# Kernel optimization log

Hardware: AMD Instinct MI355X
Metric: run time of the kernel (lower is better)

Reference implementation:

```python
import jax, jax.numpy as jnp
import numpy as np

N = 100000      # nodes
E = 1000000     # edges
H_DIM = 124     # node embedding dim
CLS_DIM = 4     # node class-logit dim (H_DIM + CLS_DIM = in_features = 128)
POLAR_DIM = 2   # edge_pred_features
HIDDEN = 256
OUT = 2
LN_EPS = 1e-5


def setup_inputs() -> dict:
    key = jax.random.key(0)
    ks = jax.random.split(key, 10)
    in_dim = 2 * (H_DIM + CLS_DIM) + POLAR_DIM  # 258
    return {
        "h": jax.random.normal(ks[0], (N, H_DIM), dtype=jnp.float32),
        "cls": jax.random.normal(ks[1], (N, CLS_DIM), dtype=jnp.float32),
        "polar": jax.random.normal(ks[2], (E, POLAR_DIM), dtype=jnp.float32),
        "src": jax.random.randint(ks[3], (E,), 0, N, dtype=jnp.int64),
        "dst": jax.random.randint(ks[4], (E,), 0, N, dtype=jnp.int64),
        # parameters (PyTorch Linear default-ish init scale)
        "W1": jax.random.normal(ks[5], (in_dim, HIDDEN), dtype=jnp.float32) * (1.0 / np.sqrt(in_dim)),
        "b1": jnp.zeros((HIDDEN,), dtype=jnp.float32),
        "gamma": jnp.ones((HIDDEN,), dtype=jnp.float32),
        "beta": jnp.zeros((HIDDEN,), dtype=jnp.float32),
        "W2": jax.random.normal(ks[6], (HIDDEN, OUT), dtype=jnp.float32) * (1.0 / np.sqrt(HIDDEN)),
        "b2": jnp.zeros((OUT,), dtype=jnp.float32),
    }


def reference(h, cls, polar, src, dst, W1, b1, gamma, beta, W2, b2):
    # softmax over class logits per node (same math as softmax on gathered
    # edge copies, but computed once per node)
    cls_sm = jax.nn.softmax(cls, axis=1)                  # [N, CLS_DIM]
    # gather src/dst node features along edges
    x = jnp.concatenate(
        [h[src], cls_sm[src], polar, h[dst], cls_sm[dst]], axis=1
    )                                                     # [E, 258]
    z = x @ W1 + b1                                        # [E, HIDDEN]
    # LayerNorm
    mu = jnp.mean(z, axis=-1, keepdims=True)
    var = jnp.mean(jnp.square(z - mu), axis=-1, keepdims=True)
    z = (z - mu) * jax.lax.rsqrt(var + LN_EPS) * gamma + beta
    z = jax.nn.relu(z)
    # dropout is identity in eval mode
    score = z @ W2 + b2                                    # [E, OUT]
    return score
```

## Files before the change

### kernel.cpp

```cpp
#include <hip/hip_runtime.h>
#include <hip/hip_bf16.h>

#define NN 100000
#define EE 1000000
#define H_DIM 124
#define PCOLS 512
#define LDK 136
#define CW 132

typedef float f32x4 __attribute__((ext_vector_type(4)));
typedef unsigned int u32x4 __attribute__((ext_vector_type(4)));
typedef short bf16x8 __attribute__((ext_vector_type(8)));
typedef _Float16 h2 __attribute__((ext_vector_type(2)));

__device__ __forceinline__ unsigned short f2bf(float f) {
    unsigned int x = __float_as_uint(f);
    unsigned int r = (x + 0x7FFFu + ((x >> 16) & 1u)) >> 16;
    return (unsigned short)r;
}
__device__ __forceinline__ unsigned int pk2bf(float a, float b) {
    return (unsigned int)f2bf(a) | ((unsigned int)f2bf(b) << 16);
}
__device__ __forceinline__ unsigned int pk2h(float a, float b) {
    h2 v = (h2){(_Float16)a, (_Float16)b};
    return __builtin_bit_cast(unsigned int, v);
}

__device__ __forceinline__ float fdot2(h2 a, h2 b, float c) {
#if __has_builtin(__builtin_amdgcn_fdot2)
    return __builtin_amdgcn_fdot2(a, b, c, false);
#else
    return c + (float)a[0] * (float)b[0] + (float)a[1] * (float)b[1];
#endif
}

#if __has_builtin(__builtin_amdgcn_update_dpp)
template <int CTRL>
__device__ __forceinline__ float dpp_add(float x) {
    int xi = __builtin_bit_cast(int, x);
    int t = __builtin_amdgcn_update_dpp(xi, xi, CTRL, 0xF, 0xF, false);
    return x + __builtin_bit_cast(float, t);
}
__device__ __forceinline__ float reduce16(float x) {
    x = dpp_add<0x128>(x);
    x = dpp_add<0x124>(x);
    x = dpp_add<0x122>(x);
    x = dpp_add<0x121>(x);
    return x;
}
#else
__device__ __forceinline__ float reduce16(float x) {
    x += __shfl_xor(x, 8); x += __shfl_xor(x, 4);
    x += __shfl_xor(x, 2); x += __shfl_xor(x, 1);
    return x;
}
#endif

__global__ __launch_bounds__(256) void build_w1t_ct(const float* __restrict__ W1,
                                                    const float* __restrict__ gamma,
                                                    const float* __restrict__ beta,
                                                    const float* __restrict__ W2,
                                                    unsigned short* __restrict__ W1T,
                                                    uint4* __restrict__ CT) {
    if (blockIdx.x < 256) {
        int t2 = blockIdx.x * 256 + threadIdx.x;
        int j = t2 >> 7, k = t2 & 127;
        int row = (j < 256) ? k : (130 + k);
        int col = (j < 256) ? j : (j - 256);
        W1T[t2] = f2bf(W1[row * 256 + col]);
    } else {
        int t = threadIdx.x;
        if (t < 192) {
            int slot = t % 12, il = t / 12;
            int a = slot >> 1, k = slot & 1;
            int j0 = il * 16 + k * 8;
            float v[8];
            #pragma unroll
            for (int i = 0; i < 8; ++i) {
                int j = j0 + i;
                v[i] = (a == 0) ? W1[128 * 256 + j]
                     : (a == 1) ? W1[129 * 256 + j]
                     : (a == 2) ? gamma[j]
                     : (a == 3) ? beta[j]
                     : (a == 4) ? W2[2 * j]
                     :            W2[2 * j + 1];
            }
            CT[t] = make_uint4(pk2h(v[0], v[1]), pk2h(v[2], v[3]),
                               pk2h(v[4], v[5]), pk2h(v[6], v[7]));
        }
    }
}

__global__ __launch_bounds__(256) void p_gemm(const float* __restrict__ h,
                                              const float* __restrict__ cls,
                                              const unsigned short* __restrict__ W1T,
                                              const float* __restrict__ b1,
                                              _Float16* __restrict__ P) {
    __shared__ alignas(16) unsigned short As[64 * LDK];
    __shared__ alignas(16) unsigned short Bs[128 * LDK];
    float* Cs = (float*)&Bs[0];
    const int m0 = blockIdx.x * 64;
    const int t = threadIdx.x;

    #pragma unroll
    for (int it = 0; it < 4; ++it) {
        int chunk = t + it * 256;
        int r = chunk >> 4, c8 = chunk & 15;
        int row = m0 + r;
        unsigned int w0 = 0, w1 = 0, w2 = 0, w3 = 0;
        if (row < NN) {
            if (c8 < 15) {
                const float* hp = h + (size_t)row * H_DIM + c8 * 8;
                float4 v0 = *(const float4*)(hp);
                float4 v1 = *(const float4*)(hp + 4);
                w0 = pk2bf(v0.x, v0.y); w1 = pk2bf(v0.z, v0.w);
                w2 = pk2bf(v1.x, v1.y); w3 = pk2bf(v1.z, v1.w);
            } else {
                float4 v0 = *(const float4*)(h + (size_t)row * H_DIM + 120);
                float4 c = *(const float4*)(cls + (size_t)row * 4);
                float m = fmaxf(fmaxf(c.x, c.y), fmaxf(c.z, c.w));
                float e0 = __expf(c.x - m), e1 = __expf(c.y - m);
                float e2 = __expf(c.z - m), e3 = __expf(c.w - m);
                float inv = 1.0f / (e0 + e1 + e2 + e3);
                w0 = pk2bf(v0.x, v0.y); w1 = pk2bf(v0.z, v0.w);
                w2 = pk2bf(e0 * inv, e1 * inv); w3 = pk2bf(e2 * inv, e3 * inv);
            }
        }
        *(uint4*)(&As[r * LDK + c8 * 8]) = make_uint4(w0, w1, w2, w3);
    }
    __syncthreads();

    const int wave = t >> 6, lane = t & 63;
    const int wm = wave & 1, wn = wave >> 1;
    const int lm = lane & 15, quad = lane >> 4;

    bf16x8 afrag[4][2];
    #pragma unroll
    for (int s = 0; s < 4; ++s) {
        int k0 = s * 32 + quad * 8;
        #pragma unroll
        for (int mt = 0; mt < 2; ++mt)
            afrag[s][mt] = *(const bf16x8*)(&As[(wm * 32 + mt * 16 + lm) * LDK + k0]);
    }

    for (int cchunk = 0; cchunk < 4; ++cchunk) {
        const int n0 = cchunk * 128;
        if (cchunk) __syncthreads();
        #pragma unroll
        for (int it = 0; it < 8; ++it) {
            int chunk = t + it * 256;
            int r = chunk >> 4, c = chunk & 15;
            float4 v = *(const float4*)(W1T + (n0 + r) * 128 + c * 8);
            *(float4*)(&Bs[r * LDK + c * 8]) = v;
        }
        __syncthreads();

        f32x4 acc[2][4];
        #pragma unroll
        for (int mt = 0; mt < 2; ++mt)
            #pragma unroll
            for (int nt = 0; nt < 4; ++nt)
                acc[mt][nt] = (f32x4){0.f, 0.f, 0.f, 0.f};

        #pragma unroll
        for (int s = 0; s < 4; ++s) {
            int k0 = s * 32 + quad * 8;
            bf16x8 b[4];
            #pragma unroll
            for (int nt = 0; nt < 4; ++nt)
                b[nt] = *(const bf16x8*)(&Bs[(wn * 64 + nt * 16 + lm) * LDK + k0]);
            #pragma unroll
            for (int mt = 0; mt < 2; ++mt)
                #pragma unroll
                for (int nt = 0; nt < 4; ++nt)
                    acc[mt][nt] = __builtin_amdgcn_mfma_f32_16x16x32_bf16(afrag[s][mt], b[nt], acc[mt][nt], 0, 0, 0);
        }
        __syncthreads();

        #pragma unroll
        for (int mt = 0; mt < 2; ++mt)
            #pragma unroll
            for (int nt = 0; nt < 4; ++nt) {
                int col = wn * 64 + nt * 16 + lm;
                int rb  = wm * 32 + mt * 16 + quad * 4;
                #pragma unroll
                for (int r = 0; r < 4; ++r)
                    Cs[(rb + r) * CW + col] = acc[mt][nt][r];
            }
        __syncthreads();

        #pragma unroll
        for (int it = 0; it < 4; ++it) {
            int chunk = t + it * 256;
            int r = chunk >> 4, c8 = chunk & 15;
            float4 a = *(const float4*)(Cs + r * CW + c8 * 8);
            float4 b = *(const float4*)(Cs + r * CW + c8 * 8 + 4);
            if (n0 >= 256) {
                int cb = n0 + c8 * 8 - 256;
                float4 ba = *(const float4*)(b1 + cb);
                float4 bb = *(const float4*)(b1 + cb + 4);
                a.x += ba.x; a.y += ba.y; a.z += ba.z; a.w += ba.w;
                b.x += bb.x; b.y += bb.y; b.z += bb.z; b.w += bb.w;
            }
            uint4 o = make_uint4(pk2h(a.x, a.y), pk2h(a.z, a.w),
                                 pk2h(b.x, b.y), pk2h(b.z, b.w));
            int row = m0 + r;
            if (row < NN)
                *(uint4*)(P + (size_t)row * PCOLS + n0 + c8 * 8) = o;
        }
    }
}

#define K3_BLOCKS 4096
#define K3_STRIDE 65536
#define K3_ROUNDS 16

__device__ __forceinline__ void stage16(const void* g, void* l) {
#if __has_builtin(__builtin_amdgcn_global_load_lds)
    __builtin_amdgcn_global_load_lds((const __attribute__((address_space(1))) void*)g,
                                     (__attribute__((address_space(3))) void*)l, 16, 0, 0);
#else
    int ln = threadIdx.x & 63;
    *(uint4*)((char*)l + ln * 16) = *(const uint4*)g;
#endif
}
__device__ __forceinline__ void stage4(const void* g, void* l) {
#if __has_builtin(__builtin_amdgcn_global_load_lds)
    __builtin_amdgcn_global_load_lds((const __attribute__((address_space(1))) void*)g,
                                     (__attribute__((address_space(3))) void*)l, 4, 0, 0);
#else
    int ln = threadIdx.x & 63;
    *(unsigned*)((char*)l + ln * 4) = *(const unsigned*)g;
#endif
}

__device__ __forceinline__ h2 pick(const u32x4& x0, const u32x4& x1, int j) {
    unsigned v = (j < 4) ? x0[j] : x1[j - 4];
    return __builtin_bit_cast(h2, v);
}

__global__ __launch_bounds__(256, 4) void edge_kernel(const _Float16* __restrict__ P,
                                                      const int* __restrict__ src,
                                                      const int* __restrict__ dst,
                                                      const float* __restrict__ polar,
                                                      const uint4* __restrict__ CT,
                                                      const float* __restrict__ b2,
                                                      float* __restrict__ out) {
    __shared__ alignas(16) char SB[4 * 8192 + 4 * 768];
    const int t    = threadIdx.x;
    const int lane = t & 63;
    const int w    = t >> 6;
    const int il   = lane & 15;
    const int g    = lane >> 4;
    const int wid  = blockIdx.x * 4 + w;
    const int ebase = wid * 4;

    char* pb = SB + w * 8192;
    char* ib = SB + 4 * 8192 + w * 768;

    uint4 cq[12];
    #pragma unroll
    for (int i = 0; i < 12; ++i) cq[i] = CT[il * 12 + i];
    h2 w0c[8], w1c[8], gc[8], bc[8], w2ac[8], w2bc[8];
    {
        const h2* ch = (const h2*)cq;
        #pragma unroll
        for (int p = 0; p < 8; ++p) {
            w0c[p]  = ch[p];      w1c[p]  = ch[8 + p];
            gc[p]   = ch[16 + p]; bc[p]   = ch[24 + p];
            w2ac[p] = ch[32 + p]; w2bc[p] = ch[40 + p];
        }
    }
    const float b20 = b2[0], b21 = b2[1];
    const h2 onep  = (h2){(_Float16)1.0f, (_Float16)1.0f};
    const h2 zerop = (h2){(_Float16)0.0f, (_Float16)0.0f};

    const int sel  = (il < 4) ? 0 : (il < 8) ? 1 : 2;
    const int eoff = (il < 4) ? il : (il < 8) ? (il - 4) : ((il - 8) >> 1);
    const int comp = (sel == 2) ? (il & 1) : 0;

    #define IDX_GADDR(rr)                                                      \
        ((sel == 0) ? (const void*)(src + (((ebase + eoff + (rr) * K3_STRIDE) < EE) ? (ebase + eoff + (rr) * K3_STRIDE) : (EE - 1))) \
       : (sel == 1) ? (const void*)(dst + (((ebase + eoff + (rr) * K3_STRIDE) < EE) ? (ebase + eoff + (rr) * K3_STRIDE) : (EE - 1))) \
       :              (const void*)(polar + 2 * (size_t)(((ebase + eoff + (rr) * K3_STRIDE) < EE) ? (ebase + eoff + (rr) * K3_STRIDE) : (EE - 1)) + comp))

    stage4(IDX_GADDR(0), ib + 0);
    asm volatile("s_waitcnt vmcnt(0)" ::: "memory");
    __builtin_amdgcn_sched_barrier(0);
    {
        const unsigned* inx = (const unsigned*)(ib + 0);
        unsigned sv = inx[g], dv = inx[4 + g];
        sv = (sv < NN) ? sv : 0u; dv = (dv < NN) ? dv : 0u;
        const char* srow = (const char*)P + ((size_t)sv << 10) + il * 32;
        const char* drow = (const char*)P + ((size_t)dv << 10) + 512 + il * 32;
        stage16(srow, pb);            stage16(srow + 16, pb + 1024);
        stage16(drow, pb + 2048);     stage16(drow + 16, pb + 3072);
    }
    stage4(IDX_GADDR(1), ib + 256);

    #pragma unroll
    for (int r = 0; r < K3_ROUNDS; ++r) {
        char* pcur = pb + (r & 1) * 4096;
        const char* icur = ib + (r % 3) * 256;
        asm volatile("s_waitcnt vmcnt(0)" ::: "memory");
        __builtin_amdgcn_sched_barrier(0);

        if (r + 1 < K3_ROUNDS) {
            const unsigned* inx = (const unsigned*)(ib + ((r + 1) % 3) * 256);
            unsigned sv = inx[g], dv = inx[4 + g];
            sv = (sv < NN) ? sv : 0u; dv = (dv < NN) ? dv : 0u;
            char* pnxt = pb + ((r + 1) & 1) * 4096;
            const char* srow = (const char*)P + ((size_t)sv << 10) + il * 32;
            const char* drow = (const char*)P + ((size_t)dv << 10) + 512 + il * 32;
            stage16(srow, pnxt);          stage16(srow + 16, pnxt + 1024);
            stage16(drow, pnxt + 2048);   stage16(drow + 16, pnxt + 3072);
        }
        if (r + 2 < K3_ROUNDS)
            stage4(IDX_GADDR(r + 2), ib + ((r + 2) % 3) * 256);

        float2 qv = *(const float2*)(icur + 32 + 8 * g);
        u32x4 a0 = *(const u32x4*)(pcur + lane * 16);
        u32x4 a1 = *(const u32x4*)(pcur + 1024 + lane * 16);
        u32x4 c0 = *(const u32x4*)(pcur + 2048 + lane * 16);
        u32x4 c1 = *(const u32x4*)(pcur + 3072 + lane * 16);

        h2 p0 = (h2){(_Float16)qv.x, (_Float16)qv.x};
        h2 p1 = (h2){(_Float16)qv.y, (_Float16)qv.y};
        h2 z[8];
        float sum = 0.f, ss = 0.f;
        #pragma unroll
        for (int p = 0; p < 8; ++p) {
            h2 pv = pick(a0, a1, p) + pick(c0, c1, p);
            h2 cc = w0c[p] * p0 + w1c[p] * p1;
            z[p] = pv + cc;
            sum = fdot2(z[p], onep, sum);
            ss  = fdot2(z[p], z[p], ss);
        }
        sum = reduce16(sum); ss = reduce16(ss);
        float mu   = sum * (1.0f / 256.0f);
        float var  = ss * (1.0f / 256.0f) - mu * mu;
        float rstd = rsqrtf(var + 1e-5f);
        float nmur = -mu * rstd;
        h2 rsh = (h2){(_Float16)rstd, (_Float16)rstd};
        h2 nmh = (h2){(_Float16)nmur, (_Float16)nmur};
        float o0 = 0.f, o1 = 0.f;
        #pragma unroll
        for (int p = 0; p < 8; ++p) {
            h2 tt = z[p] * rsh + nmh;
            h2 u  = tt * gc[p] + bc[p];
            u = __builtin_elementwise_max(u, zerop);
            o0 = fdot2(u, w2ac[p], o0);
            o1 = fdot2(u, w2bc[p], o1);
        }
        o0 = reduce16(o0); o1 = reduce16(o1);
        int eg = ebase + g + r * K3_STRIDE;
        if (il == 0 && eg < EE)
            *(float2*)(out + 2 * (size_t)eg) = make_float2(o0 + b20, o1 + b21);
    }
    #undef IDX_GADDR
}

extern "C" void kernel_launch(void* const* d_in, const int* in_sizes, int n_in,
                              void* d_out, int out_size, void* d_ws, size_t ws_size,
                              hipStream_t stream) {
    const float* h     = (const float*)d_in[0];
    const float* cls   = (const float*)d_in[1];
    const float* polar = (const float*)d_in[2];
    const int*   src   = (const int*)d_in[3];
    const int*   dst   = (const int*)d_in[4];
    const float* W1    = (const float*)d_in[5];
    const float* b1    = (const float*)d_in[6];
    const float* gamma = (const float*)d_in[7];
    const float* beta  = (const float*)d_in[8];
    const float* W2    = (const float*)d_in[9];
    const float* b2    = (const float*)d_in[10];
    float* out = (float*)d_out;

    char* ws = (char*)d_ws;
    _Float16*       P   = (_Float16*)ws;
    unsigned short* W1T = (unsigned short*)(ws + 102400000);
    uint4*          CT  = (uint4*)(ws + 102531072);

    build_w1t_ct<<<257, 256, 0, stream>>>(W1, gamma, beta, W2, W1T, CT);
    p_gemm<<<1563, 256, 0, stream>>>(h, cls, W1T, b1, P);
    edge_kernel<<<K3_BLOCKS, 256, 0, stream>>>(P, src, dst, polar, CT, b2, out);
}
```

Measured before the change: 290.1 us.

## Deepen edge gather pipeline to triple-buffered rows and five-deep index prefetch

The edge kernel's async LDS staging goes from double-buffered gathered rows and a 3-slot index ring to triple-buffered rows and a 5-slot index ring. Loads are issued two rounds ahead for rows and four rounds ahead for indices. The full vmcnt(0) wait is replaced by partial waits, so more global gathers stay in flight while a round computes. In exchange, per-wave LDS grows and launch bounds drop from 4 to 3 blocks per CU, which lowers occupancy; the exact vmcnt counts also depend on how output stores are ordered.

```diff
diff --git a/kernel.cpp b/kernel.cpp
--- a/kernel.cpp
+++ b/kernel.cpp
@@ -214,6 +214,7 @@
 #define K3_BLOCKS 4096
 #define K3_STRIDE 65536
 #define K3_ROUNDS 16
+#define PWB 13568
 
 __device__ __forceinline__ void stage16(const void* g, void* l) {
 #if __has_builtin(__builtin_amdgcn_global_load_lds)
@@ -239,14 +240,14 @@
     return __builtin_bit_cast(h2, v);
 }
 
-__global__ __launch_bounds__(256, 4) void edge_kernel(const _Float16* __restrict__ P,
+__global__ __launch_bounds__(256, 3) void edge_kernel(const _Float16* __restrict__ P,
                                                       const int* __restrict__ src,
                                                       const int* __restrict__ dst,
                                                       const float* __restrict__ polar,
                                                       const uint4* __restrict__ CT,
                                                       const float* __restrict__ b2,
                                                       float* __restrict__ out) {
-    __shared__ alignas(16) char SB[4 * 8192 + 4 * 768];
+    __shared__ alignas(16) char SB[4 * PWB];
     const int t    = threadIdx.x;
     const int lane = t & 63;
     const int w    = t >> 6;
@@ -255,8 +256,8 @@
     const int wid  = blockIdx.x * 4 + w;
     const int ebase = wid * 4;
 
-    char* pb = SB + w * 8192;
-    char* ib = SB + 4 * 8192 + w * 768;
+    char* pb = SB + w * PWB;
+    char* ib = pb + 12288;
 
     uint4 cq[12];
     #pragma unroll
@@ -284,40 +285,37 @@
        : (sel == 1) ? (const void*)(dst + (((ebase + eoff + (rr) * K3_STRIDE) < EE) ? (ebase + eoff + (rr) * K3_STRIDE) : (EE - 1))) \
        :              (const void*)(polar + 2 * (size_t)(((ebase + eoff + (rr) * K3_STRIDE) < EE) ? (ebase + eoff + (rr) * K3_STRIDE) : (EE - 1)) + comp))
 
-    stage4(IDX_GADDR(0), ib + 0);
+    #define ISSUE_P(j) {                                                       \
+        const unsigned* inx = (const unsigned*)(ib + ((j) % 5) * 256);         \
+        unsigned sv = inx[g], dv = inx[4 + g];                                 \
+        sv = (sv < NN) ? sv : 0u; dv = (dv < NN) ? dv : 0u;                    \
+        char* pn = pb + ((j) % 3) * 4096;                                      \
+        const char* srow = (const char*)P + ((size_t)sv << 10) + il * 32;      \
+        const char* drow = (const char*)P + ((size_t)dv << 10) + 512 + il * 32;\
+        stage16(srow, pn);          stage16(srow + 16, pn + 1024);             \
+        stage16(drow, pn + 2048);   stage16(drow + 16, pn + 3072); }
+
+    stage4(IDX_GADDR(0), ib + 0 * 256);
+    stage4(IDX_GADDR(1), ib + 1 * 256);
     asm volatile("s_waitcnt vmcnt(0)" ::: "memory");
     __builtin_amdgcn_sched_barrier(0);
-    {
-        const unsigned* inx = (const unsigned*)(ib + 0);
-        unsigned sv = inx[g], dv = inx[4 + g];
-        sv = (sv < NN) ? sv : 0u; dv = (dv < NN) ? dv : 0u;
-        const char* srow = (const char*)P + ((size_t)sv << 10) + il * 32;
-        const char* drow = (const char*)P + ((size_t)dv << 10) + 512 + il * 32;
-        stage16(srow, pb);            stage16(srow + 16, pb + 1024);
-        stage16(drow, pb + 2048);     stage16(drow + 16, pb + 3072);
-    }
-    stage4(IDX_GADDR(1), ib + 256);
+    ISSUE_P(0);
+    stage4(IDX_GADDR(2), ib + 2 * 256);
+    ISSUE_P(1);
+    stage4(IDX_GADDR(3), ib + 3 * 256);
 
     #pragma unroll
     for (int r = 0; r < K3_ROUNDS; ++r) {
-        char* pcur = pb + (r & 1) * 4096;
-        const char* icur = ib + (r % 3) * 256;
-        asm volatile("s_waitcnt vmcnt(0)" ::: "memory");
+        if (r == 0)       { asm volatile("s_waitcnt vmcnt(5)" ::: "memory"); }
+        else if (r == 15) { asm volatile("s_waitcnt vmcnt(2)" ::: "memory"); }
+        else              { asm volatile("s_waitcnt vmcnt(6)" ::: "memory"); }
         __builtin_amdgcn_sched_barrier(0);
 
-        if (r + 1 < K3_ROUNDS) {
-            const unsigned* inx = (const unsigned*)(ib + ((r + 1) % 3) * 256);
-            unsigned sv = inx[g], dv = inx[4 + g];
-            sv = (sv < NN) ? sv : 0u; dv = (dv < NN) ? dv : 0u;
-            char* pnxt = pb + ((r + 1) & 1) * 4096;
-            const char* srow = (const char*)P + ((size_t)sv << 10) + il * 32;
-            const char* drow = (const char*)P + ((size_t)dv << 10) + 512 + il * 32;
-            stage16(srow, pnxt);          stage16(srow + 16, pnxt + 1024);
-            stage16(drow, pnxt + 2048);   stage16(drow + 16, pnxt + 3072);
-        }
-        if (r + 2 < K3_ROUNDS)
-            stage4(IDX_GADDR(r + 2), ib + ((r + 2) % 3) * 256);
-
+        if (r + 2 < K3_ROUNDS) ISSUE_P(r + 2);
+        if (r + 4 < K3_ROUNDS) stage4(IDX_GADDR(r + 4), ib + ((r + 4) % 5) * 256);
+
+        const char* pcur = pb + (r % 3) * 4096;
+        const char* icur = ib + (r % 5) * 256;
         float2 qv = *(const float2*)(icur + 32 + 8 * g);
         u32x4 a0 = *(const u32x4*)(pcur + lane * 16);
         u32x4 a1 = *(const u32x4*)(pcur + 1024 + lane * 16);
@@ -357,7 +355,9 @@
         if (il == 0 && eg < EE)
             *(float2*)(out + 2 * (size_t)eg) = make_float2(o0 + b20, o1 + b21);
     }
+    #undef ISSUE_P
     #undef IDX_GADDR
+    asm volatile("s_waitcnt vmcnt(0)" ::: "memory");
 }
 
 extern "C" void kernel_launch(void* const* d_in, const int* in_sizes, int n_in,
```

Result: slower. 304.1 us (+4.8%).
